# Performance work log

Measured on AMD Instinct MI355X. Metric: run time of the kernel, lower is better.

Reference implementation:

```python
import jax, jax.numpy as jnp
import numpy as np

T = 65536
DIN = 128
H = 128      # hidden_dim
L = 16       # latent_dim
NEG_SLOPE = 0.01  # flax nn.leaky_relu default


def _orth(key, shape, scale):
    a = jax.random.normal(key, shape, dtype=jnp.float32)
    q, r = jnp.linalg.qr(a if shape[0] >= shape[1] else a.T)
    q = q * jnp.sign(jnp.diag(r))
    q = q if shape[0] >= shape[1] else q.T
    return (scale * q[:shape[0], :shape[1]]).astype(jnp.float32)


def setup_inputs() -> dict:
    key = jax.random.key(0)
    ks = jax.random.split(key, 8)
    x = jax.random.normal(ks[0], (T, DIN), dtype=jnp.float32)
    mask = jax.random.bernoulli(ks[1], 0.9, (T,))
    W_in = _orth(ks[2], (DIN, H), float(np.sqrt(2.0)))
    b_in = jnp.zeros((H,), jnp.float32)
    # OptimizedLSTMCell params: input kernel [DIN_h, 4H], recurrent kernel [H, 4H], bias [4H]
    # gate order in flax: i, f, g, o
    Wi = jax.random.normal(ks[3], (H, 4 * H), dtype=jnp.float32) / np.sqrt(H)
    Wh = _orth(ks[4], (H, 4 * H), 1.0)
    b_lstm = jnp.zeros((4 * H,), jnp.float32)
    W_lat = _orth(ks[5], (H, L), 1.0)
    b_lat = jnp.zeros((L,), jnp.float32)
    return {"x": x, "mask": mask, "W_in": W_in, "b_in": b_in,
            "Wi": Wi, "Wh": Wh, "b_lstm": b_lstm,
            "W_lat": W_lat, "b_lat": b_lat}


def reference(x, mask, W_in, b_in, Wi, Wh, b_lstm, W_lat, b_lat):
    # input projection + leaky_relu
    xp = x @ W_in + b_in                      # [T, H]
    xp = jnp.where(xp >= 0, xp, NEG_SLOPE * xp)

    def step(carry, inp):
        c, h = carry
        xt, mt = inp
        z = xt @ Wi + h @ Wh + b_lstm         # [4H]
        i, f, g, o = jnp.split(z, 4)
        c_new = jax.nn.sigmoid(f) * c + jax.nn.sigmoid(i) * jnp.tanh(g)
        h_new = jax.nn.sigmoid(o) * jnp.tanh(c_new)
        # masked carry update: keep old carry where mask is False
        c2 = jnp.where(mt, c_new, c)
        h2 = jnp.where(mt, h_new, h)
        return (c2, h2), h_new

    init = (jnp.zeros((H,), xp.dtype), jnp.zeros((H,), xp.dtype))
    (c_f, h_f), _ = jax.lax.scan(step, init, (xp, mask))
    latent = h_f @ W_lat + b_lat              # [L]
    return latent
```

## Files before the change

kernel.cpp:

```cpp
#include <hip/hip_runtime.h>
#include <hip/hip_fp16.h>


#define TT   65536
#define DINN 128
#define HH   128
#define G4   512
#define NEG  0.01f
#define ROWS 16
#define CTH  1024

#define SC_SIG  (-1.4426950408889634f)
#define SC_TANH ( 2.8853900817779268f)

typedef _Float16 f16x8 __attribute__((ext_vector_type(8)));
typedef float    f32x4 __attribute__((ext_vector_type(4)));

#if defined(__has_builtin)
#if __has_builtin(__builtin_amdgcn_rcpf)
#define RCPF(x) __builtin_amdgcn_rcpf(x)
#endif
#if __has_builtin(__builtin_amdgcn_exp2f)
#define EXP2F(x) __builtin_amdgcn_exp2f(x)
#endif
#endif
#ifndef RCPF
#define RCPF(x) (1.0f / (x))
#endif
#ifndef EXP2F
#define EXP2F(x) exp2f(x)
#endif

#define MF16(a, b, c) __builtin_amdgcn_mfma_f32_16x16x32_f16((a), (b), (c), 0, 0, 0)

#define LDS_BARRIER() asm volatile("s_waitcnt lgkmcnt(0)\n\ts_barrier" ::: "memory")

__global__ __launch_bounds__(CTH) void compact_kernel(
    const int* __restrict__ mask, int* __restrict__ pos, int* __restrict__ cnt_out)
{
    __shared__ int sc[CTH];
    const int th   = threadIdx.x;
    const int base = th * (TT / CTH);
    int cnt = 0;
    #pragma unroll 8
    for (int k = 0; k < TT / CTH; ++k) cnt += (mask[base + k] != 0);
    sc[th] = cnt;
    __syncthreads();
    for (int off = 1; off < CTH; off <<= 1) {
        int v = sc[th];
        int u = (th >= off) ? sc[th - off] : 0;
        __syncthreads();
        sc[th] = v + u;
        __syncthreads();
    }
    int p = sc[th] - cnt;
    for (int k = 0; k < TT / CTH; ++k) {
        int t = base + k;
        pos[t] = p;
        p += (mask[t] != 0);
    }
    if (th == CTH - 1) cnt_out[0] = sc[CTH - 1];
}

__global__ __launch_bounds__(512) void zx_kernel(
    const float* __restrict__ x, const float* __restrict__ W_in,
    const float* __restrict__ b_in, const float* __restrict__ Wi,
    const float* __restrict__ b_lstm, const int* __restrict__ mask,
    const int* __restrict__ pos, __half* __restrict__ zc)
{
    __shared__ float xt[ROWS][DINN];
    __shared__ float xp[ROWS][DINN];
    const int tid = threadIdx.x;
    const int t0  = blockIdx.x * ROWS;

    {
        const float4* src = (const float4*)(x + (size_t)t0 * DINN);
        ((float4*)&xt[0][0])[tid] = src[tid];
    }
    __syncthreads();

    {
        const int c  = tid & 127;
        const int r0 = tid >> 7;
        float a0 = b_in[c], a1 = a0, a2 = a0, a3 = a0;
        #pragma unroll
        for (int k4 = 0; k4 < DINN / 4; ++k4) {
            const float w0 = W_in[(k4*4+0)*DINN + c];
            const float w1 = W_in[(k4*4+1)*DINN + c];
            const float w2 = W_in[(k4*4+2)*DINN + c];
            const float w3 = W_in[(k4*4+3)*DINN + c];
            float4 v0 = *(const float4*)&xt[r0 +  0][k4*4];
            float4 v1 = *(const float4*)&xt[r0 +  4][k4*4];
            float4 v2 = *(const float4*)&xt[r0 +  8][k4*4];
            float4 v3 = *(const float4*)&xt[r0 + 12][k4*4];
            a0 += v0.x*w0 + v0.y*w1 + v0.z*w2 + v0.w*w3;
            a1 += v1.x*w0 + v1.y*w1 + v1.z*w2 + v1.w*w3;
            a2 += v2.x*w0 + v2.y*w1 + v2.z*w2 + v2.w*w3;
            a3 += v3.x*w0 + v3.y*w1 + v3.z*w2 + v3.w*w3;
        }
        xp[r0 +  0][c] = a0 >= 0.f ? a0 : NEG * a0;
        xp[r0 +  4][c] = a1 >= 0.f ? a1 : NEG * a1;
        xp[r0 +  8][c] = a2 >= 0.f ? a2 : NEG * a2;
        xp[r0 + 12][c] = a3 >= 0.f ? a3 : NEG * a3;
    }
    __syncthreads();

    {
        const int c2 = tid;
        float acc[ROWS];
        const float bl = b_lstm[c2];
        #pragma unroll
        for (int r = 0; r < ROWS; ++r) acc[r] = bl;
        #pragma unroll 4
        for (int k4 = 0; k4 < DINN / 4; ++k4) {
            const float w0 = Wi[(k4*4+0)*G4 + c2];
            const float w1 = Wi[(k4*4+1)*G4 + c2];
            const float w2 = Wi[(k4*4+2)*G4 + c2];
            const float w3 = Wi[(k4*4+3)*G4 + c2];
            #pragma unroll
            for (int r = 0; r < ROWS; ++r) {
                float4 a = *(const float4*)&xp[r][k4*4];
                acc[r] += a.x*w0 + a.y*w1 + a.z*w2 + a.w*w3;
            }
        }
        const int   gate = c2 >> 7;
        const int   unit = c2 & 127;
        const int   dst  = (unit >> 5) * 128 + (unit & 15) * 8
                         + ((unit >> 4) & 1) * 4 + gate;
        const float gsc  = (gate == 2) ? SC_TANH : SC_SIG;
        #pragma unroll
        for (int r = 0; r < ROWS; ++r) {
            const int t = t0 + r;
            if (mask[t])
                zc[(size_t)pos[t] * G4 + dst] = __float2half(acc[r] * gsc);
        }
    }
}

#define DBW(g,a,kt) f16x8 bw##g##_##a##_##kt;
#define LBW(g,a,kt) { f16x8 v_;                                            \
    const float sc_ = ((g) == 2) ? SC_TANH : SC_SIG;                       \
    const int col_ = ((g) << 7) + (w << 5) + ((a) << 4) + li;              \
    _Pragma("unroll")                                                      \
    for (int j_ = 0; j_ < 8; ++j_)                                         \
        v_[j_] = (_Float16)(Wh[((kt)*32 + r8 + j_)*G4 + col_] * sc_);      \
    bw##g##_##a##_##kt = v_; }
#define PBW(g,a,kt) asm volatile("" : "+v"(bw##g##_##a##_##kt));

#define FORKT(M,g,a) M(g,a,0) M(g,a,1) M(g,a,2) M(g,a,3)
#define FORA(M,g)    FORKT(M,g,0) FORKT(M,g,1)
#define FORALLB(M)   FORA(M,0) FORA(M,1) FORA(M,2) FORA(M,3)

#define CHAIN(g,a,zout) {                                             \
    f32x4 d_ = MF16(af0, bw##g##_##a##_0, zq);                        \
    d_ = MF16(af1, bw##g##_##a##_1, d_);                              \
    d_ = MF16(af2, bw##g##_##a##_2, d_);                              \
    d_ = MF16(af3, bw##g##_##a##_3, d_);                              \
    (zout) = d_[0]; }

#define STEP(ZZ, PI, PO) {                                            \
    const __half2 zl = *(const __half2*)&(ZZ).x;                      \
    const __half2 zh = *(const __half2*)&(ZZ).y;                      \
    const __half* hb_ = hbuf[PI];                                     \
    const f16x8 af0 = *(const f16x8*)&hb_[ 0 + r8];                   \
    const f16x8 af1 = *(const f16x8*)&hb_[32 + r8];                   \
    const f16x8 af2 = *(const f16x8*)&hb_[64 + r8];                   \
    const f16x8 af3 = *(const f16x8*)&hb_[96 + r8];                   \
    float z00, z01, z10, z11, z20, z21, z30, z31;                     \
    CHAIN(0,0,z00) CHAIN(0,1,z01)                                     \
    CHAIN(1,0,z10) CHAIN(1,1,z11)                                     \
    CHAIN(2,0,z20) CHAIN(2,1,z21)                                     \
    CHAIN(3,0,z30) CHAIN(3,1,z31)                                     \
    const float zi = (asel ? z01 : z00) + __half2float(zl.x);         \
    const float zf = (asel ? z11 : z10) + __half2float(zl.y);         \
    const float zg = (asel ? z21 : z20) + __half2float(zh.x);         \
    const float zo = (asel ? z31 : z30) + __half2float(zh.y);         \
    const float i_s = RCPF(1.f + EXP2F(zi));                          \
    const float f_s = RCPF(1.f + EXP2F(zf));                          \
    const float o_s = RCPF(1.f + EXP2F(zo));                          \
    const float g_t = 1.f - 2.f * RCPF(EXP2F(zg) + 1.f);              \
    c_st = f_s * c_st + i_s * g_t;                                    \
    const float t_c = 1.f - 2.f * RCPF(EXP2F(SC_TANH * c_st) + 1.f);  \
    h_st = o_s * t_c;                                                 \
    if (wr) hbuf[PO][uout] = __float2half(h_st);                      \
    LDS_BARRIER();                                                    \
}

__global__ __launch_bounds__(256, 1)
__attribute__((amdgpu_waves_per_eu(1, 1)))
void scan_kernel(
    const __half* __restrict__ zc, const float* __restrict__ Wh,
    const int* __restrict__ cnt, const float* __restrict__ W_lat,
    const float* __restrict__ b_lat, float* __restrict__ out)
{
    const int n    = threadIdx.x;
    const int w    = n >> 6;
    const int lane = n & 63;
    const int li   = lane & 15;
    const int r    = lane >> 4;
    const int r8   = r << 3;
    const bool asel = (r & 1);
    const bool wr   = (r < 2);
    const int uout  = (w << 5) + (r << 4) + li;

    FORALLB(DBW)
    FORALLB(LBW)
    FORALLB(PBW)

    f32x4 zq = { 0.f, 0.f, 0.f, 0.f };
    asm volatile("" : "+v"(zq));

    __shared__ __align__(16) __half hbuf[2][HH];
    __shared__ float hfin[HH];
    ((__half*)hbuf)[n] = __float2half(0.f);
    float c_st = 0.f, h_st = 0.f;
    __syncthreads();

    const int S = cnt[0];
    const uint2* prow = (const uint2*)zc + (w << 5) + (li << 1) + (int)asel;
    uint2 z0 = prow[0];
    uint2 z1 = prow[128];
    prow += 256;

    int i = 0;
    for (; i + 1 < S; i += 2) {
        const uint2 za = prow[0];
        const uint2 zb = prow[128];
        prow += 256;
        STEP(z0, 0, 1)
        STEP(z1, 1, 0)
        z0 = za;
        z1 = zb;
    }
    if (i < S) {
        STEP(z0, 0, 1)
    }

    if (wr) hfin[uout] = h_st;
    __syncthreads();
    if (n < 16) {
        float acc = b_lat[n];
        #pragma unroll
        for (int k = 0; k < HH; ++k) acc += hfin[k] * W_lat[k * 16 + n];
        out[n] = acc;
    }
}

extern "C" void kernel_launch(void* const* d_in, const int* in_sizes, int n_in,
                              void* d_out, int out_size, void* d_ws, size_t ws_size,
                              hipStream_t stream) {
    const float* x      = (const float*)d_in[0];
    const int*   mask   = (const int*)  d_in[1];
    const float* W_in   = (const float*)d_in[2];
    const float* b_in   = (const float*)d_in[3];
    const float* Wi     = (const float*)d_in[4];
    const float* Wh     = (const float*)d_in[5];
    const float* b_lstm = (const float*)d_in[6];
    const float* W_lat  = (const float*)d_in[7];
    const float* b_lat  = (const float*)d_in[8];
    float* out = (float*)d_out;

    __half* zc  = (__half*)d_ws;
    int*    pos = (int*)((char*)d_ws + (size_t)(TT + 4) * G4 * 2);
    int*    cnt = pos + TT;

    compact_kernel<<<1, CTH, 0, stream>>>(mask, pos, cnt);
    zx_kernel<<<TT / ROWS, 512, 0, stream>>>(x, W_in, b_in, Wi, b_lstm,
                                             mask, pos, zc);
    scan_kernel<<<1, 256, 0, stream>>>(zc, Wh, cnt, W_lat, b_lat, out);
}
```

Measured before the change: 23.12 ms.

## Replace MFMA recurrent matvec with per-thread dot2 over 512 threads

The sequential LSTM scan stops using chains of 16x16x32 MFMA instructions, which wasted most of their output, and instead gives each of 512 threads one gate column. Each thread does a 128-long fp16 dot product with v_dot2_f32_f16, keeping its Wh column in registers. Gate values are exchanged across lanes with shuffles so every unit's lane holds i, f, g and o. The aim is to shorten the per-step critical latency of the serial recurrence. The cost is a 512-thread barrier each step, extra shuffles, and reading each zx gate as a single 16-bit load.

```diff
diff --git a/kernel.cpp b/kernel.cpp
--- a/kernel.cpp
+++ b/kernel.cpp
@@ -13,8 +13,10 @@
 #define SC_SIG  (-1.4426950408889634f)
 #define SC_TANH ( 2.8853900817779268f)
 
-typedef _Float16 f16x8 __attribute__((ext_vector_type(8)));
-typedef float    f32x4 __attribute__((ext_vector_type(4)));
+typedef unsigned int u32;
+typedef unsigned short u16;
+typedef u32 u32x4 __attribute__((ext_vector_type(4)));
+typedef _Float16 h2v __attribute__((ext_vector_type(2)));
 
 #if defined(__has_builtin)
 #if __has_builtin(__builtin_amdgcn_rcpf)
@@ -30,8 +32,6 @@
 #ifndef EXP2F
 #define EXP2F(x) exp2f(x)
 #endif
-
-#define MF16(a, b, c) __builtin_amdgcn_mfma_f32_16x16x32_f16((a), (b), (c), 0, 0, 0)
 
 #define LDS_BARRIER() asm volatile("s_waitcnt lgkmcnt(0)\n\ts_barrier" ::: "memory")
 
@@ -137,57 +137,59 @@
     }
 }
 
-#define DBW(g,a,kt) f16x8 bw##g##_##a##_##kt;
-#define LBW(g,a,kt) { f16x8 v_;                                            \
-    const float sc_ = ((g) == 2) ? SC_TANH : SC_SIG;                       \
-    const int col_ = ((g) << 7) + (w << 5) + ((a) << 4) + li;              \
+#define DW(j) u32x4 wf##j;
+#define LW(j) { u32x4 t_;                                                  \
     _Pragma("unroll")                                                      \
-    for (int j_ = 0; j_ < 8; ++j_)                                         \
-        v_[j_] = (_Float16)(Wh[((kt)*32 + r8 + j_)*G4 + col_] * sc_);      \
-    bw##g##_##a##_##kt = v_; }
-#define PBW(g,a,kt) asm volatile("" : "+v"(bw##g##_##a##_##kt));
-
-#define FORKT(M,g,a) M(g,a,0) M(g,a,1) M(g,a,2) M(g,a,3)
-#define FORA(M,g)    FORKT(M,g,0) FORKT(M,g,1)
-#define FORALLB(M)   FORA(M,0) FORA(M,1) FORA(M,2) FORA(M,3)
-
-#define CHAIN(g,a,zout) {                                             \
-    f32x4 d_ = MF16(af0, bw##g##_##a##_0, zq);                        \
-    d_ = MF16(af1, bw##g##_##a##_1, d_);                              \
-    d_ = MF16(af2, bw##g##_##a##_2, d_);                              \
-    d_ = MF16(af3, bw##g##_##a##_3, d_);                              \
-    (zout) = d_[0]; }
-
-#define STEP(ZZ, PI, PO) {                                            \
-    const __half2 zl = *(const __half2*)&(ZZ).x;                      \
-    const __half2 zh = *(const __half2*)&(ZZ).y;                      \
-    const __half* hb_ = hbuf[PI];                                     \
-    const f16x8 af0 = *(const f16x8*)&hb_[ 0 + r8];                   \
-    const f16x8 af1 = *(const f16x8*)&hb_[32 + r8];                   \
-    const f16x8 af2 = *(const f16x8*)&hb_[64 + r8];                   \
-    const f16x8 af3 = *(const f16x8*)&hb_[96 + r8];                   \
-    float z00, z01, z10, z11, z20, z21, z30, z31;                     \
-    CHAIN(0,0,z00) CHAIN(0,1,z01)                                     \
-    CHAIN(1,0,z10) CHAIN(1,1,z11)                                     \
-    CHAIN(2,0,z20) CHAIN(2,1,z21)                                     \
-    CHAIN(3,0,z30) CHAIN(3,1,z31)                                     \
-    const float zi = (asel ? z01 : z00) + __half2float(zl.x);         \
-    const float zf = (asel ? z11 : z10) + __half2float(zl.y);         \
-    const float zg = (asel ? z21 : z20) + __half2float(zh.x);         \
-    const float zo = (asel ? z31 : z30) + __half2float(zh.y);         \
-    const float i_s = RCPF(1.f + EXP2F(zi));                          \
-    const float f_s = RCPF(1.f + EXP2F(zf));                          \
-    const float o_s = RCPF(1.f + EXP2F(zo));                          \
-    const float g_t = 1.f - 2.f * RCPF(EXP2F(zg) + 1.f);              \
-    c_st = f_s * c_st + i_s * g_t;                                    \
-    const float t_c = 1.f - 2.f * RCPF(EXP2F(SC_TANH * c_st) + 1.f);  \
-    h_st = o_s * t_c;                                                 \
-    if (wr) hbuf[PO][uout] = __float2half(h_st);                      \
-    LDS_BARRIER();                                                    \
-}
-
-__global__ __launch_bounds__(256, 1)
-__attribute__((amdgpu_waves_per_eu(1, 1)))
+    for (int m_ = 0; m_ < 4; ++m_) {                                       \
+        h2v p_;                                                            \
+        p_[0] = (_Float16)(Wh[((j)*8 + 2*m_ + 0)*G4 + col] * scW);         \
+        p_[1] = (_Float16)(Wh[((j)*8 + 2*m_ + 1)*G4 + col] * scW);         \
+        t_[m_] = __builtin_bit_cast(u32, p_);                              \
+    }                                                                      \
+    wf##j = t_; }
+#define PW(j) asm volatile("" : "+v"(wf##j));
+
+#define FORJ16(M) M(0) M(1) M(2) M(3) M(4) M(5) M(6) M(7) \
+                  M(8) M(9) M(10) M(11) M(12) M(13) M(14) M(15)
+
+#define LH(j) const u32x4 hq##j = hb4_[j];
+
+#define DOTF(j, A) {                                                       \
+    asm("v_dot2_f32_f16 %0, %1, %2, %0" : "+v"(A) : "v"(hq##j[0]), "v"(wf##j[0])); \
+    asm("v_dot2_f32_f16 %0, %1, %2, %0" : "+v"(A) : "v"(hq##j[1]), "v"(wf##j[1])); \
+    asm("v_dot2_f32_f16 %0, %1, %2, %0" : "+v"(A) : "v"(hq##j[2]), "v"(wf##j[2])); \
+    asm("v_dot2_f32_f16 %0, %1, %2, %0" : "+v"(A) : "v"(hq##j[3]), "v"(wf##j[3])); }
+
+#define STEP(ZV, PI, PO) {                                                 \
+    const u32x4* hb4_ = (const u32x4*)hbuf[PI];                            \
+    LH(0) LH(1) LH(2)  LH(3)  LH(4)  LH(5)  LH(6)  LH(7)                   \
+    LH(8) LH(9) LH(10) LH(11) LH(12) LH(13) LH(14) LH(15)                  \
+    float a0 = __half2float(__builtin_bit_cast(__half, (u16)(ZV)));        \
+    float a1 = 0.f, a2 = 0.f, a3 = 0.f;                                    \
+    DOTF(0,a0)  DOTF(1,a1)  DOTF(2,a2)  DOTF(3,a3)                         \
+    DOTF(4,a0)  DOTF(5,a1)  DOTF(6,a2)  DOTF(7,a3)                         \
+    DOTF(8,a0)  DOTF(9,a1)  DOTF(10,a2) DOTF(11,a3)                        \
+    DOTF(12,a0) DOTF(13,a1) DOTF(14,a2) DOTF(15,a3)                        \
+    const float z_ = (a0 + a1) + (a2 + a3);                                \
+    const float e_ = EXP2F(z_);                                            \
+    const float r_ = RCPF(1.f + e_);                                       \
+    const float nl = isg2 ? 1.f - 2.f * r_ : r_;                           \
+    const float x16 = __shfl_xor(nl, 16, 64);                              \
+    const float x32 = __shfl_xor(nl, 32, 64);                              \
+    const float x48 = __shfl_xor(nl, 48, 64);                              \
+    const float i_s = b5 ? (b4 ? x48 : x32) : (b4 ? x16 : nl);             \
+    const float f_s = b5 ? (b4 ? x32 : x48) : (b4 ? nl  : x16);            \
+    const float g_t = b5 ? (b4 ? x16 : nl)  : (b4 ? x48 : x32);            \
+    const float o_s = b5 ? (b4 ? nl  : x16) : (b4 ? x32 : x48);            \
+    c_st = f_s * c_st + i_s * g_t;                                         \
+    const float ec_ = EXP2F(SC_TANH * c_st);                               \
+    h_st = o_s * (1.f - 2.f * RCPF(ec_ + 1.f));                            \
+    if (wrh) hbuf[PO][u] = __float2half(h_st);                             \
+    LDS_BARRIER();                                                         \
+}
+
+__global__ __launch_bounds__(512, 2)
+__attribute__((amdgpu_waves_per_eu(2, 2)))
 void scan_kernel(
     const __half* __restrict__ zc, const float* __restrict__ Wh,
     const int* __restrict__ cnt, const float* __restrict__ W_lat,
@@ -196,37 +198,38 @@
     const int n    = threadIdx.x;
     const int w    = n >> 6;
     const int lane = n & 63;
-    const int li   = lane & 15;
-    const int r    = lane >> 4;
-    const int r8   = r << 3;
-    const bool asel = (r & 1);
-    const bool wr   = (r < 2);
-    const int uout  = (w << 5) + (r << 4) + li;
-
-    FORALLB(DBW)
-    FORALLB(LBW)
-    FORALLB(PBW)
-
-    f32x4 zq = { 0.f, 0.f, 0.f, 0.f };
-    asm volatile("" : "+v"(zq));
+    const int ul   = lane & 15;
+    const int g    = lane >> 4;
+    const bool b4  = (lane >> 4) & 1;
+    const bool b5  = (lane >> 5) & 1;
+    const bool isg2 = (g == 2);
+    const bool wrh  = (g == 0);
+    const int u    = (w << 4) + ul;
+    const int col  = (g << 7) + u;
+    const float scW = isg2 ? SC_TANH : SC_SIG;
+
+    FORJ16(DW)
+    FORJ16(LW)
+    FORJ16(PW)
 
     __shared__ __align__(16) __half hbuf[2][HH];
     __shared__ float hfin[HH];
-    ((__half*)hbuf)[n] = __float2half(0.f);
+    if (n < 256) ((__half*)hbuf)[n] = __float2half(0.f);
     float c_st = 0.f, h_st = 0.f;
     __syncthreads();
 
     const int S = cnt[0];
-    const uint2* prow = (const uint2*)zc + (w << 5) + (li << 1) + (int)asel;
-    uint2 z0 = prow[0];
-    uint2 z1 = prow[128];
-    prow += 256;
+    const int dst = (u >> 5) * 128 + (u & 15) * 8 + ((u >> 4) & 1) * 4 + g;
+    const u16* pz = (const u16*)zc + dst;
+    u16 z0 = pz[0];
+    u16 z1 = pz[512];
+    pz += 1024;
 
     int i = 0;
     for (; i + 1 < S; i += 2) {
-        const uint2 za = prow[0];
-        const uint2 zb = prow[128];
-        prow += 256;
+        const u16 za = pz[0];
+        const u16 zb = pz[512];
+        pz += 1024;
         STEP(z0, 0, 1)
         STEP(z1, 1, 0)
         z0 = za;
@@ -236,7 +239,7 @@
         STEP(z0, 0, 1)
     }
 
-    if (wr) hfin[uout] = h_st;
+    if (wrh) hfin[u] = h_st;
     __syncthreads();
     if (n < 16) {
         float acc = b_lat[n];
@@ -267,5 +270,5 @@
     compact_kernel<<<1, CTH, 0, stream>>>(mask, pos, cnt);
     zx_kernel<<<TT / ROWS, 512, 0, stream>>>(x, W_in, b_in, Wi, b_lstm,
                                              mask, pos, zc);
-    scan_kernel<<<1, 256, 0, stream>>>(zc, Wh, cnt, W_lat, b_lat, out);
-}
+    scan_kernel<<<1, 512, 0, stream>>>(zc, Wh, cnt, W_lat, b_lat, out);
+}
```

Result: slower. 36.84 ms (+59.3%).

## Replace MFMA recurrent matvec with per-lane v_dot2 FMA chains and shuffle reduction

Applied to the files above, without the earlier changes.

The serial LSTM recurrence previously computed h@Wh with chains of 16x16x32 MFMAs in which only one column of each output tile was used, so most of the matrix work was wasted and each step waited on long MFMA dependency chains. Each lane now holds 128 packed f16 weight pairs for one hidden unit and half of K. It computes all four gates with v_dot2_f32_f16 instructions and combines the two K halves with a cross-half shuffle. This trades MFMA latency for many VALU dot instructions plus a DPP/shuffle reduction per step, and puts heavy register pressure on each lane.

```diff
diff --git a/kernel.cpp b/kernel.cpp
--- a/kernel.cpp
+++ b/kernel.cpp
@@ -13,8 +13,10 @@
 #define SC_SIG  (-1.4426950408889634f)
 #define SC_TANH ( 2.8853900817779268f)
 
-typedef _Float16 f16x8 __attribute__((ext_vector_type(8)));
-typedef float    f32x4 __attribute__((ext_vector_type(4)));
+typedef unsigned int u32;
+typedef unsigned short u16;
+typedef u32 u32x4 __attribute__((ext_vector_type(4)));
+typedef _Float16 h2v __attribute__((ext_vector_type(2)));
 
 #if defined(__has_builtin)
 #if __has_builtin(__builtin_amdgcn_rcpf)
@@ -30,8 +32,6 @@
 #ifndef EXP2F
 #define EXP2F(x) exp2f(x)
 #endif
-
-#define MF16(a, b, c) __builtin_amdgcn_mfma_f32_16x16x32_f16((a), (b), (c), 0, 0, 0)
 
 #define LDS_BARRIER() asm volatile("s_waitcnt lgkmcnt(0)\n\ts_barrier" ::: "memory")
 
@@ -137,53 +137,59 @@
     }
 }
 
-#define DBW(g,a,kt) f16x8 bw##g##_##a##_##kt;
-#define LBW(g,a,kt) { f16x8 v_;                                            \
+#define DWG(g,j) u32x4 wg##g##_##j;
+#define LWG(g,j) { u32x4 t_;                                               \
     const float sc_ = ((g) == 2) ? SC_TANH : SC_SIG;                       \
-    const int col_ = ((g) << 7) + (w << 5) + ((a) << 4) + li;              \
+    const int col_ = ((g) << 7) + u;                                       \
     _Pragma("unroll")                                                      \
-    for (int j_ = 0; j_ < 8; ++j_)                                         \
-        v_[j_] = (_Float16)(Wh[((kt)*32 + r8 + j_)*G4 + col_] * sc_);      \
-    bw##g##_##a##_##kt = v_; }
-#define PBW(g,a,kt) asm volatile("" : "+v"(bw##g##_##a##_##kt));
-
-#define FORKT(M,g,a) M(g,a,0) M(g,a,1) M(g,a,2) M(g,a,3)
-#define FORA(M,g)    FORKT(M,g,0) FORKT(M,g,1)
-#define FORALLB(M)   FORA(M,0) FORA(M,1) FORA(M,2) FORA(M,3)
-
-#define CHAIN(g,a,zout) {                                             \
-    f32x4 d_ = MF16(af0, bw##g##_##a##_0, zq);                        \
-    d_ = MF16(af1, bw##g##_##a##_1, d_);                              \
-    d_ = MF16(af2, bw##g##_##a##_2, d_);                              \
-    d_ = MF16(af3, bw##g##_##a##_3, d_);                              \
-    (zout) = d_[0]; }
-
-#define STEP(ZZ, PI, PO) {                                            \
-    const __half2 zl = *(const __half2*)&(ZZ).x;                      \
-    const __half2 zh = *(const __half2*)&(ZZ).y;                      \
-    const __half* hb_ = hbuf[PI];                                     \
-    const f16x8 af0 = *(const f16x8*)&hb_[ 0 + r8];                   \
-    const f16x8 af1 = *(const f16x8*)&hb_[32 + r8];                   \
-    const f16x8 af2 = *(const f16x8*)&hb_[64 + r8];                   \
-    const f16x8 af3 = *(const f16x8*)&hb_[96 + r8];                   \
-    float z00, z01, z10, z11, z20, z21, z30, z31;                     \
-    CHAIN(0,0,z00) CHAIN(0,1,z01)                                     \
-    CHAIN(1,0,z10) CHAIN(1,1,z11)                                     \
-    CHAIN(2,0,z20) CHAIN(2,1,z21)                                     \
-    CHAIN(3,0,z30) CHAIN(3,1,z31)                                     \
-    const float zi = (asel ? z01 : z00) + __half2float(zl.x);         \
-    const float zf = (asel ? z11 : z10) + __half2float(zl.y);         \
-    const float zg = (asel ? z21 : z20) + __half2float(zh.x);         \
-    const float zo = (asel ? z31 : z30) + __half2float(zh.y);         \
-    const float i_s = RCPF(1.f + EXP2F(zi));                          \
-    const float f_s = RCPF(1.f + EXP2F(zf));                          \
-    const float o_s = RCPF(1.f + EXP2F(zo));                          \
-    const float g_t = 1.f - 2.f * RCPF(EXP2F(zg) + 1.f);              \
-    c_st = f_s * c_st + i_s * g_t;                                    \
-    const float t_c = 1.f - 2.f * RCPF(EXP2F(SC_TANH * c_st) + 1.f);  \
-    h_st = o_s * t_c;                                                 \
-    if (wr) hbuf[PO][uout] = __float2half(h_st);                      \
-    LDS_BARRIER();                                                    \
+    for (int m_ = 0; m_ < 4; ++m_) {                                       \
+        h2v p_;                                                            \
+        p_[0] = (_Float16)(Wh[(K0 + (j)*8 + 2*m_ + 0)*G4 + col_] * sc_);   \
+        p_[1] = (_Float16)(Wh[(K0 + (j)*8 + 2*m_ + 1)*G4 + col_] * sc_);   \
+        t_[m_] = __builtin_bit_cast(u32, p_);                              \
+    }                                                                      \
+    wg##g##_##j = t_; }
+#define PWG(g,j) asm volatile("" : "+v"(wg##g##_##j));
+
+#define FORJ(M,g)  M(g,0) M(g,1) M(g,2) M(g,3) M(g,4) M(g,5) M(g,6) M(g,7)
+#define FORALLW(M) FORJ(M,0) FORJ(M,1) FORJ(M,2) FORJ(M,3)
+
+#define DOTM(j,m) {                                                        \
+    asm("v_dot2_f32_f16 %0, %1, %2, %0" : "+v"(a0) : "v"(hq##j[m]), "v"(wg0_##j[m])); \
+    asm("v_dot2_f32_f16 %0, %1, %2, %0" : "+v"(a1) : "v"(hq##j[m]), "v"(wg1_##j[m])); \
+    asm("v_dot2_f32_f16 %0, %1, %2, %0" : "+v"(a2) : "v"(hq##j[m]), "v"(wg2_##j[m])); \
+    asm("v_dot2_f32_f16 %0, %1, %2, %0" : "+v"(a3) : "v"(hq##j[m]), "v"(wg3_##j[m])); }
+#define DOTJ(j) DOTM(j,0) DOTM(j,1) DOTM(j,2) DOTM(j,3)
+
+#define SWADD(a) { (a) += __shfl_xor((a), 32, 64); }
+
+#define STEP(ZZ, PI, PO) {                                                 \
+    const __half2 zl = *(const __half2*)&(ZZ).x;                \
+    const __half2 zh = *(const __half2*)&(ZZ).y;                \
+    const u32x4* hb4_ = (const u32x4*)&hbuf[PI][K0];                       \
+    const u32x4 hq0 = hb4_[0];                                             \
+    const u32x4 hq1 = hb4_[1];                                             \
+    const u32x4 hq2 = hb4_[2];                                             \
+    const u32x4 hq3 = hb4_[3];                                             \
+    const u32x4 hq4 = hb4_[4];                                             \
+    const u32x4 hq5 = hb4_[5];                                             \
+    const u32x4 hq6 = hb4_[6];                                             \
+    const u32x4 hq7 = hb4_[7];                                             \
+    float a0 = kh0 ? __half2float(zl.x) : 0.f;                             \
+    float a1 = kh0 ? __half2float(zl.y) : 0.f;                             \
+    float a2 = kh0 ? __half2float(zh.x) : 0.f;                             \
+    float a3 = kh0 ? __half2float(zh.y) : 0.f;                             \
+    DOTJ(0) DOTJ(1) DOTJ(2) DOTJ(3) DOTJ(4) DOTJ(5) DOTJ(6) DOTJ(7)       \
+    SWADD(a0) SWADD(a1) SWADD(a2) SWADD(a3)                                \
+    const float i_s = RCPF(1.f + EXP2F(a0));                               \
+    const float f_s = RCPF(1.f + EXP2F(a1));                               \
+    const float g_t = 1.f - 2.f * RCPF(EXP2F(a2) + 1.f);                   \
+    const float o_s = RCPF(1.f + EXP2F(a3));                               \
+    c_st = f_s * c_st + i_s * g_t;                                         \
+    const float t_c = 1.f - 2.f * RCPF(EXP2F(SC_TANH * c_st) + 1.f);       \
+    h_st = o_s * t_c;                                                      \
+    if (kh0) hbuf[PO][u] = __float2half(h_st);                             \
+    LDS_BARRIER();                                                         \
 }
 
 __global__ __launch_bounds__(256, 1)
@@ -196,19 +202,15 @@
     const int n    = threadIdx.x;
     const int w    = n >> 6;
     const int lane = n & 63;
-    const int li   = lane & 15;
-    const int r    = lane >> 4;
-    const int r8   = r << 3;
-    const bool asel = (r & 1);
-    const bool wr   = (r < 2);
-    const int uout  = (w << 5) + (r << 4) + li;
-
-    FORALLB(DBW)
-    FORALLB(LBW)
-    FORALLB(PBW)
-
-    f32x4 zq = { 0.f, 0.f, 0.f, 0.f };
-    asm volatile("" : "+v"(zq));
+    const int ulo  = lane & 31;
+    const int kh   = lane >> 5;
+    const bool kh0 = (kh == 0);
+    const int u    = (w << 5) + ulo;
+    const int K0   = kh << 6;
+
+    FORALLW(DWG)
+    FORALLW(LWG)
+    FORALLW(PWG)
 
     __shared__ __align__(16) __half hbuf[2][HH];
     __shared__ float hfin[HH];
@@ -217,7 +219,8 @@
     __syncthreads();
 
     const int S = cnt[0];
-    const uint2* prow = (const uint2*)zc + (w << 5) + (li << 1) + (int)asel;
+    const uint2* prow = (const uint2*)zc + (w << 5) + ((ulo & 15) << 1)
+                      + ((ulo >> 4) & 1);
     uint2 z0 = prow[0];
     uint2 z1 = prow[128];
     prow += 256;
@@ -236,7 +239,7 @@
         STEP(z0, 0, 1)
     }
 
-    if (wr) hfin[uout] = h_st;
+    if (kh0) hfin[u] = h_st;
     __syncthreads();
     if (n < 16) {
         float acc = b_lat[n];
```

New measurement: 32.25 ms. +39.5%, slower.
